# Optimization experiments

Hardware: AMD Instinct MI355X
Metric: run time of the kernel (lower is better)

Reference implementation:

```python
import jax, jax.numpy as jnp
import numpy as np

B, N, T, L = 4, 512, 288, 128
NEG_SLOPE = 0.2
TEMPERATURE = 0.2
CLAMP = 10.0
EPS = 1e-10


def setup_inputs() -> dict:
    key = jax.random.key(0)
    ks = jax.random.split(key, 6)
    s_in = 1.0 / np.sqrt(T)
    s_lat = 1.0 / np.sqrt(2 * L)
    s_b = 1.0 / np.sqrt(L)
    x = jax.random.normal(ks[0], (B, N, T), dtype=jnp.float32)
    W1 = jax.random.normal(ks[1], (L, T), dtype=jnp.float32) * s_in
    W2 = jax.random.normal(ks[2], (L, T), dtype=jnp.float32) * s_in
    Wp = jax.random.normal(ks[3], (L, 2 * L), dtype=jnp.float32) * s_lat
    Wb = jax.random.normal(ks[4], (L,), dtype=jnp.float32) * s_b
    noise = jnp.clip(jax.random.uniform(ks[5], (N, N), dtype=jnp.float32), 1e-6, 1.0 - 1e-6)
    return {
        "x": x,
        "W1": W1, "b1": jnp.zeros((L,), jnp.float32),
        "W2": W2, "b2": jnp.zeros((L,), jnp.float32),
        "Wp": Wp, "bp": jnp.zeros((L,), jnp.float32),
        "Wb": Wb, "bb": jnp.zeros((1,), jnp.float32),
        "noise": noise,
    }


def _leaky(v):
    return jnp.where(v >= 0, v, NEG_SLOPE * v)


def reference(x, W1, b1, W2, b2, Wp, bp, Wb, bb, noise):
    # per-node projections (B, N, L)
    x1 = _leaky(jnp.einsum('bnt,lt->bnl', x, W1) + b1)
    x2 = _leaky(jnp.einsum('bnt,lt->bnl', x, W2) + b2)
    # linear_para_latent(cat(x1_i, x2_j)) == x1_i @ Wp_a^T + x2_j @ Wp_b^T + bp
    Wp_a, Wp_b = Wp[:, :L], Wp[:, L:]
    s1 = jnp.einsum('bnl,ml->bnm', x1, Wp_a)  # (B, N, L_out)
    s2 = jnp.einsum('bnl,ml->bnm', x2, Wp_b)
    pair = s1[:, :, None, :] + s2[:, None, :, :] + bp  # (B, N, N, L)
    h = _leaky(pair)
    logits = jnp.einsum('bijl,l->bij', h, Wb) + bb[0]  # (B, N, N)
    p = jax.nn.sigmoid(logits).mean(axis=0)            # (N, N)
    p = p * (1.0 - jnp.eye(N, dtype=p.dtype))          # fill_diagonal_(0)
    # relaxed Bernoulli sample (binary concrete) with logit clamping
    logit_p = jnp.clip(jnp.log(p + EPS) - jnp.log1p(-p + EPS), -CLAMP, CLAMP)
    logistic = jnp.log(noise) - jnp.log1p(-noise)
    adj = jax.nn.sigmoid((logit_p + logistic) / TEMPERATURE)
    return adj
```

## Files before the change

### kernel.cpp

```cpp
#include <hip/hip_runtime.h>
#include <hip/hip_bf16.h>
#include <math.h>

#define NN 512
#define NT 288

__global__ __launch_bounds__(512) void kP(
    const float* __restrict__ x,
    const float* __restrict__ W1,
    const float* __restrict__ b1,
    const float* __restrict__ W2,
    const float* __restrict__ b2,
    const float* __restrict__ Wp,
    const float* __restrict__ bp,
    const float* __restrict__ Wb,
    const float* __restrict__ bb,
    float* __restrict__ S12,
    float* __restrict__ Aarr,
    float* __restrict__ Carr)
{
    __shared__ __align__(16) float xs[8 * NT];
    __shared__ __align__(16) float x12s[8 * 256];
    __shared__ __align__(16) float ph[8 * 256];

    const int t   = threadIdx.x;
    const int bn0 = blockIdx.x * 8;
    const int col = t & 255;
    const int kh  = t >> 8;

    for (int q = 0; q < 2; ++q) {
        int idx = q * 512 + t;
        if (idx < 576) {
            int row = idx / 72, c4 = idx % 72;
            *(float4*)&xs[row * NT + c4 * 4] =
                *(const float4*)&x[(size_t)(bn0 + row) * NT + c4 * 4];
        }
    }
    __syncthreads();

    const float* wrow = ((col < 128) ? (W1 + col * NT) : (W2 + (col - 128) * NT))
                        + kh * 144;
    const float bias1 = (col < 128) ? b1[col] : b2[col - 128];
    const int kb1 = kh * 144;

    float acc[8];
#pragma unroll
    for (int n = 0; n < 8; ++n) acc[n] = 0.0f;

    for (int k = 0; k < 144; k += 4) {
        float4 w = *(const float4*)(wrow + k);
#pragma unroll
        for (int n = 0; n < 8; ++n) {
            float4 xv = *(const float4*)&xs[n * NT + kb1 + k];
            acc[n] = fmaf(w.x, xv.x, acc[n]);
            acc[n] = fmaf(w.y, xv.y, acc[n]);
            acc[n] = fmaf(w.z, xv.z, acc[n]);
            acc[n] = fmaf(w.w, xv.w, acc[n]);
        }
    }
    if (kh) {
#pragma unroll
        for (int n = 0; n < 8; ++n) ph[n * 256 + col] = acc[n];
    }
    __syncthreads();
    if (!kh) {
#pragma unroll
        for (int n = 0; n < 8; ++n) {
            float v = acc[n] + ph[n * 256 + col] + bias1;
            x12s[n * 256 + col] = fmaxf(v, 0.2f * v);
        }
    }
    __syncthreads();

    const int koff = (col < 128) ? 0 : 128;
    const float* wprow = ((col < 128) ? (Wp + col * 256) : (Wp + (col - 128) * 256 + 128))
                         + kh * 64;
    const float bias2 = (col < 128) ? bp[col] : 0.0f;
    const int kb2 = koff + kh * 64;

    float acc2[8];
#pragma unroll
    for (int n = 0; n < 8; ++n) acc2[n] = 0.0f;

    for (int k = 0; k < 64; k += 4) {
        float4 w = *(const float4*)(wprow + k);
#pragma unroll
        for (int n = 0; n < 8; ++n) {
            float4 xv = *(const float4*)&x12s[n * 256 + kb2 + k];
            acc2[n] = fmaf(w.x, xv.x, acc2[n]);
            acc2[n] = fmaf(w.y, xv.y, acc2[n]);
            acc2[n] = fmaf(w.z, xv.z, acc2[n]);
            acc2[n] = fmaf(w.w, xv.w, acc2[n]);
        }
    }
    if (kh) {
#pragma unroll
        for (int n = 0; n < 8; ++n) ph[n * 256 + col] = acc2[n];
    }
    __syncthreads();

    float* s12s = xs;
    if (!kh) {
#pragma unroll
        for (int n = 0; n < 8; ++n) {
            float sv = acc2[n] + ph[n * 256 + col] + bias2;
            S12[(size_t)(bn0 + n) * 256 + col] = sv;
            s12s[n * 257 + col] = sv;
        }
    }
    __syncthreads();

    {
        int lane32 = t & 31;
        int n = (t >> 5) & 7;
        int isC = t >> 8;
        int base = isC ? 128 : 0;
        float sum = 0.0f;
#pragma unroll
        for (int s = 0; s < 4; ++s) {
            int j = lane32 + s * 32;
            sum = fmaf(s12s[n * 257 + base + j], Wb[j], sum);
        }
#pragma unroll
        for (int m = 16; m >= 1; m >>= 1)
            sum += __shfl_xor(sum, m, 32);
        if (lane32 == 0) {
            if (isC) Carr[bn0 + n] = 0.6f * sum;
            else     Aarr[bn0 + n] = 0.6f * sum + bb[0];
        }
    }
}

__global__ __launch_bounds__(512) void kQ(
    const float* __restrict__ S12,
    const float* __restrict__ Aarr,
    const float* __restrict__ Carr,
    const float* __restrict__ Wb,
    const float* __restrict__ noise,
    float* __restrict__ out)
{
    __shared__ __align__(16) float smem[32768];
    float* S1t = smem;
    float* S2t = smem + 16384;

    const int t = threadIdx.x;
    const int bx = blockIdx.x, by = blockIdx.y;

#pragma unroll
    for (int q = 0; q < 16; ++q) {
        int task = q * 512 + t;
        int isS2 = task >> 12;
        int r    = task & 4095;
        int bz   = r >> 10;
        int row  = (r >> 5) & 31;
        int c4   = r & 31;
        size_t src = (size_t)(bz * NN + (isS2 ? by : bx) * 32 + row) * 256
                     + (isS2 ? 128 : 0) + c4 * 4;
        float4 v = *(const float4*)&S12[src];
        float* dst = (isS2 ? S2t : S1t) + bz * 4096;
        int rw = row ^ ((c4 & 7) << 2);
        dst[(c4 * 4 + 0) * 32 + rw] = v.x;
        dst[(c4 * 4 + 1) * 32 + rw] = v.y;
        dst[(c4 * 4 + 2) * 32 + rw] = v.z;
        dst[(c4 * 4 + 3) * 32 + rw] = v.w;
    }
    __syncthreads();

    const int lh = t >> 8;
    const int bz = (t >> 6) & 3;
    const int s  = t & 63;
    const int i0 = (s >> 3) << 2, j0 = (s & 7) << 2;

    const float* S1b = S1t + bz * 4096 + lh * 64 * 32;
    const float* S2b = S2t + bz * 4096 + lh * 64 * 32;
    const float* wbp = Wb + lh * 64;

    float accv[16];
#pragma unroll
    for (int k = 0; k < 16; ++k) accv[k] = 0.0f;

    for (int l4 = 0; l4 < 16; ++l4) {
        const int sw = (l4 & 7) << 2;
        const int lrow = l4 * 4 * 32;
        float4 wv = *(const float4*)&wbp[l4 * 4];
        const float wl[4] = {wv.x, wv.y, wv.z, wv.w};
#pragma unroll
        for (int d = 0; d < 4; ++d) {
            float4 a = *(const float4*)&S1b[lrow + d * 32 + (i0 ^ sw)];
            float4 b = *(const float4*)&S2b[lrow + d * 32 + (j0 ^ sw)];
            float w = wl[d];
            float ai[4] = {a.x, a.y, a.z, a.w};
            float bj[4] = {b.x, b.y, b.z, b.w};
#pragma unroll
            for (int ii = 0; ii < 4; ++ii)
#pragma unroll
                for (int jj = 0; jj < 4; ++jj) {
                    float tv = ai[ii] + bj[jj];
                    accv[ii * 4 + jj] = fmaf(fabsf(tv), w, accv[ii * 4 + jj]);
                }
        }
    }

    float* red = smem;
    const int tid2 = t & 255;
    __syncthreads();
    if (lh) {
#pragma unroll
        for (int q = 0; q < 4; ++q) {
            float4 v = {accv[4 * q], accv[4 * q + 1], accv[4 * q + 2], accv[4 * q + 3]};
            *(float4*)&red[q * 1024 + tid2 * 4] = v;
        }
    }
    __syncthreads();

    float sig[16];
    if (!lh) {
#pragma unroll
        for (int q = 0; q < 4; ++q) {
            float4 v = *(const float4*)&red[q * 1024 + tid2 * 4];
            accv[4 * q]     += v.x;
            accv[4 * q + 1] += v.y;
            accv[4 * q + 2] += v.z;
            accv[4 * q + 3] += v.w;
        }
        float Av[4], Cv[4];
#pragma unroll
        for (int ii = 0; ii < 4; ++ii) Av[ii] = Aarr[bz * NN + bx * 32 + i0 + ii];
#pragma unroll
        for (int jj = 0; jj < 4; ++jj) Cv[jj] = Carr[bz * NN + by * 32 + j0 + jj];
#pragma unroll
        for (int ii = 0; ii < 4; ++ii)
#pragma unroll
            for (int jj = 0; jj < 4; ++jj) {
                float lg = Av[ii] + Cv[jj] + 0.4f * accv[ii * 4 + jj];
                sig[ii * 4 + jj] = 1.0f / (1.0f + expf(-lg));
            }
        float* redB = smem + 4096;
        if (bz) {
#pragma unroll
            for (int q = 0; q < 4; ++q) {
                float4 v = {sig[4 * q], sig[4 * q + 1], sig[4 * q + 2], sig[4 * q + 3]};
                *(float4*)&redB[(bz - 1) * 1024 + q * 256 + s * 4] = v;
            }
        }
    }
    __syncthreads();

    float* redB = smem + 4096;
    float* redP = smem + 7168;
    if (t < 64) {
#pragma unroll
        for (int bzz = 0; bzz < 3; ++bzz)
#pragma unroll
            for (int q = 0; q < 4; ++q) {
                float4 v = *(const float4*)&redB[bzz * 1024 + q * 256 + t * 4];
                sig[4 * q]     += v.x;
                sig[4 * q + 1] += v.y;
                sig[4 * q + 2] += v.z;
                sig[4 * q + 3] += v.w;
            }
#pragma unroll
        for (int q = 0; q < 4; ++q) {
            float4 v = {sig[4 * q], sig[4 * q + 1], sig[4 * q + 2], sig[4 * q + 3]};
            *(float4*)&redP[t * 16 + q * 4] = v;
        }
    }
    __syncthreads();

    if (t < 256) {
        int i   = t >> 3;
        int j0f = (t & 7) * 4;
        int sP  = (t >> 5) * 8 + (t & 7);
        int k0  = ((t >> 3) & 3) * 4;
        float4 pv4 = *(const float4*)&redP[sP * 16 + k0];
        float pv[4] = {pv4.x, pv4.y, pv4.z, pv4.w};

        int gi = bx * 32 + i;
        size_t base = (size_t)gi * NN + by * 32 + j0f;
        float4 nz = *(const float4*)&noise[base];
        float nv[4] = {nz.x, nz.y, nz.z, nz.w};

        float4 o;
        float* op = (float*)&o;
#pragma unroll
        for (int c = 0; c < 4; ++c) {
            float p = 0.25f * pv[c];
            int gj = by * 32 + j0f + c;
            if (gj == gi) p = 0.0f;
            float lp = logf(p + 1e-10f) - log1pf(-p + 1e-10f);
            lp = fminf(fmaxf(lp, -10.0f), 10.0f);
            float lgs = logf(nv[c]) - log1pf(-nv[c]);
            op[c] = 1.0f / (1.0f + expf(-(lp + lgs) * 5.0f));
        }
        *(float4*)&out[base] = o;
    }
}

extern "C" void kernel_launch(void* const* d_in, const int* in_sizes, int n_in,
                              void* d_out, int out_size, void* d_ws, size_t ws_size,
                              hipStream_t stream) {
    const float* x     = (const float*)d_in[0];
    const float* W1    = (const float*)d_in[1];
    const float* b1    = (const float*)d_in[2];
    const float* W2    = (const float*)d_in[3];
    const float* b2    = (const float*)d_in[4];
    const float* Wp    = (const float*)d_in[5];
    const float* bp    = (const float*)d_in[6];
    const float* Wb    = (const float*)d_in[7];
    const float* bb    = (const float*)d_in[8];
    const float* noise = (const float*)d_in[9];

    float* ws   = (float*)d_ws;
    float* S12  = ws;
    float* Aarr = ws + 524288;
    float* Carr = Aarr + 2048;

    kP<<<256, 512, 0, stream>>>(x, W1, b1, W2, b2, Wp, bp, Wb, bb,
                                S12, Aarr, Carr);
    kQ<<<dim3(16, 16), 512, 0, stream>>>(S12, Aarr, Carr, Wb, noise,
                                         (float*)d_out);
}
```

Measured before the change: 43.62 us.

## Pre-transpose projection weights for coalesced loads and read x directly from global

Adds a small kernel that transposes W1/W2 and the two halves of Wp into k-major layouts in workspace. The projection loops in kP can then load weights coalesced across threads instead of as per-thread strided float4 rows. The shared-memory staging of x is removed, and x is read as wavefront-uniform float4 loads straight from global memory. The cost is an extra kernel launch and a transpose pass on every call, plus x reads that now go through cache rather than LDS.

```diff
diff --git a/kernel.cpp b/kernel.cpp
--- a/kernel.cpp
+++ b/kernel.cpp
@@ -5,13 +5,29 @@
 #define NN 512
 #define NT 288
 
+__global__ __launch_bounds__(256) void kT(
+    const float* __restrict__ W1, const float* __restrict__ W2,
+    const float* __restrict__ Wp,
+    float* __restrict__ Wt, float* __restrict__ Wpt)
+{
+    int g = blockIdx.x * 256 + threadIdx.x;
+    if (g < 288 * 256) {
+        int k = g >> 8, col = g & 255;
+        Wt[g] = (col < 128) ? W1[col * 288 + k] : W2[(col - 128) * 288 + k];
+    } else {
+        int h = g - 288 * 256;
+        int k = h >> 8, col = h & 255;
+        Wpt[h] = (col < 128) ? Wp[col * 256 + k]
+                             : Wp[(col - 128) * 256 + 128 + k];
+    }
+}
+
 __global__ __launch_bounds__(512) void kP(
     const float* __restrict__ x,
-    const float* __restrict__ W1,
+    const float* __restrict__ Wt,
     const float* __restrict__ b1,
-    const float* __restrict__ W2,
     const float* __restrict__ b2,
-    const float* __restrict__ Wp,
+    const float* __restrict__ Wpt,
     const float* __restrict__ bp,
     const float* __restrict__ Wb,
     const float* __restrict__ bb,
@@ -19,45 +35,38 @@
     float* __restrict__ Aarr,
     float* __restrict__ Carr)
 {
-    __shared__ __align__(16) float xs[8 * NT];
     __shared__ __align__(16) float x12s[8 * 256];
     __shared__ __align__(16) float ph[8 * 256];
+    __shared__ __align__(16) float s12s[8 * 257];
 
     const int t   = threadIdx.x;
     const int bn0 = blockIdx.x * 8;
     const int col = t & 255;
     const int kh  = t >> 8;
 
-    for (int q = 0; q < 2; ++q) {
-        int idx = q * 512 + t;
-        if (idx < 576) {
-            int row = idx / 72, c4 = idx % 72;
-            *(float4*)&xs[row * NT + c4 * 4] =
-                *(const float4*)&x[(size_t)(bn0 + row) * NT + c4 * 4];
-        }
-    }
-    __syncthreads();
-
-    const float* wrow = ((col < 128) ? (W1 + col * NT) : (W2 + (col - 128) * NT))
-                        + kh * 144;
+    const float* xb  = x + (size_t)bn0 * NT + kh * 144;
+    const float* wtb = Wt + kh * 144 * 256 + col;
+
+    float acc[8];
+#pragma unroll
+    for (int n = 0; n < 8; ++n) acc[n] = 0.0f;
+
+    for (int k4 = 0; k4 < 36; ++k4) {
+        float w0 = wtb[(k4 * 4 + 0) * 256];
+        float w1 = wtb[(k4 * 4 + 1) * 256];
+        float w2 = wtb[(k4 * 4 + 2) * 256];
+        float w3 = wtb[(k4 * 4 + 3) * 256];
+#pragma unroll
+        for (int n = 0; n < 8; ++n) {
+            float4 xv = *(const float4*)&xb[n * NT + k4 * 4];
+            acc[n] = fmaf(w0, xv.x, acc[n]);
+            acc[n] = fmaf(w1, xv.y, acc[n]);
+            acc[n] = fmaf(w2, xv.z, acc[n]);
+            acc[n] = fmaf(w3, xv.w, acc[n]);
+        }
+    }
+
     const float bias1 = (col < 128) ? b1[col] : b2[col - 128];
-    const int kb1 = kh * 144;
-
-    float acc[8];
-#pragma unroll
-    for (int n = 0; n < 8; ++n) acc[n] = 0.0f;
-
-    for (int k = 0; k < 144; k += 4) {
-        float4 w = *(const float4*)(wrow + k);
-#pragma unroll
-        for (int n = 0; n < 8; ++n) {
-            float4 xv = *(const float4*)&xs[n * NT + kb1 + k];
-            acc[n] = fmaf(w.x, xv.x, acc[n]);
-            acc[n] = fmaf(w.y, xv.y, acc[n]);
-            acc[n] = fmaf(w.z, xv.z, acc[n]);
-            acc[n] = fmaf(w.w, xv.w, acc[n]);
-        }
-    }
     if (kh) {
 #pragma unroll
         for (int n = 0; n < 8; ++n) ph[n * 256 + col] = acc[n];
@@ -73,33 +82,34 @@
     __syncthreads();
 
     const int koff = (col < 128) ? 0 : 128;
-    const float* wprow = ((col < 128) ? (Wp + col * 256) : (Wp + (col - 128) * 256 + 128))
-                         + kh * 64;
+    const float* wptb = Wpt + kh * 64 * 256 + col;
+    const int kb2 = koff + kh * 64;
+
+    float acc2[8];
+#pragma unroll
+    for (int n = 0; n < 8; ++n) acc2[n] = 0.0f;
+
+    for (int k4 = 0; k4 < 16; ++k4) {
+        float w0 = wptb[(k4 * 4 + 0) * 256];
+        float w1 = wptb[(k4 * 4 + 1) * 256];
+        float w2 = wptb[(k4 * 4 + 2) * 256];
+        float w3 = wptb[(k4 * 4 + 3) * 256];
+#pragma unroll
+        for (int n = 0; n < 8; ++n) {
+            float4 xv = *(const float4*)&x12s[n * 256 + kb2 + k4 * 4];
+            acc2[n] = fmaf(w0, xv.x, acc2[n]);
+            acc2[n] = fmaf(w1, xv.y, acc2[n]);
+            acc2[n] = fmaf(w2, xv.z, acc2[n]);
+            acc2[n] = fmaf(w3, xv.w, acc2[n]);
+        }
+    }
+
     const float bias2 = (col < 128) ? bp[col] : 0.0f;
-    const int kb2 = koff + kh * 64;
-
-    float acc2[8];
-#pragma unroll
-    for (int n = 0; n < 8; ++n) acc2[n] = 0.0f;
-
-    for (int k = 0; k < 64; k += 4) {
-        float4 w = *(const float4*)(wprow + k);
-#pragma unroll
-        for (int n = 0; n < 8; ++n) {
-            float4 xv = *(const float4*)&x12s[n * 256 + kb2 + k];
-            acc2[n] = fmaf(w.x, xv.x, acc2[n]);
-            acc2[n] = fmaf(w.y, xv.y, acc2[n]);
-            acc2[n] = fmaf(w.z, xv.z, acc2[n]);
-            acc2[n] = fmaf(w.w, xv.w, acc2[n]);
-        }
-    }
     if (kh) {
 #pragma unroll
         for (int n = 0; n < 8; ++n) ph[n * 256 + col] = acc2[n];
     }
     __syncthreads();
-
-    float* s12s = xs;
     if (!kh) {
 #pragma unroll
         for (int n = 0; n < 8; ++n) {
@@ -314,8 +324,11 @@
     float* S12  = ws;
     float* Aarr = ws + 524288;
     float* Carr = Aarr + 2048;
-
-    kP<<<256, 512, 0, stream>>>(x, W1, b1, W2, b2, Wp, bp, Wb, bb,
+    float* Wt   = Carr + 2048;
+    float* Wpt  = Wt + 73728;
+
+    kT<<<416, 256, 0, stream>>>(W1, W2, Wp, Wt, Wpt);
+    kP<<<256, 512, 0, stream>>>(x, Wt, b1, b2, Wpt, bp, Wb, bb,
                                 S12, Aarr, Carr);
     kQ<<<dim3(16, 16), 512, 0, stream>>>(S12, Aarr, Carr, Wb, noise,
                                          (float*)d_out);
```

Measured after the change: 105.1 us. 141% more time.

## Pre-transpose weights for coalesced loads and split pair kernel across 1024 threads

Applied to the files above, without the earlier changes.

Adds a kernel that rearranges W1/W2 and Wp into a k4-major interleaved layout, so each thread's float4 weight load in kP is coalesced across columns. kP now reads x and the intermediate x12 straight from global memory (x12 goes through a global scratch buffer) instead of staging them in shared memory. kQ moves to 1024 threads, splitting the latent reduction four ways instead of two, with a wider shared-memory reduction. This costs an extra launch and transposes the weights on every call, and adds global round trips for x12.

```diff
diff --git a/kernel.cpp b/kernel.cpp
--- a/kernel.cpp
+++ b/kernel.cpp
@@ -5,59 +5,69 @@
 #define NN 512
 #define NT 288
 
+__global__ __launch_bounds__(256) void kT(
+    const float* __restrict__ W1, const float* __restrict__ W2,
+    const float* __restrict__ Wp,
+    float* __restrict__ Wt2, float* __restrict__ Wpt2)
+{
+    int g = blockIdx.x * 256 + threadIdx.x;
+    if (g < 73728) {
+        int k4 = g >> 10, col = (g >> 2) & 255, d = g & 3;
+        int k = k4 * 4 + d;
+        Wt2[g] = (col < 128) ? W1[col * 288 + k] : W2[(col - 128) * 288 + k];
+    } else {
+        int h = g - 73728;
+        int k4 = h >> 10, col = (h >> 2) & 255, d = h & 3;
+        int k = k4 * 4 + d;
+        Wpt2[h] = (col < 128) ? Wp[col * 256 + k]
+                              : Wp[(col - 128) * 256 + 128 + k];
+    }
+}
+
 __global__ __launch_bounds__(512) void kP(
     const float* __restrict__ x,
-    const float* __restrict__ W1,
+    const float* __restrict__ Wt2,
     const float* __restrict__ b1,
-    const float* __restrict__ W2,
     const float* __restrict__ b2,
-    const float* __restrict__ Wp,
+    const float* __restrict__ Wpt2,
     const float* __restrict__ bp,
     const float* __restrict__ Wb,
     const float* __restrict__ bb,
     float* __restrict__ S12,
     float* __restrict__ Aarr,
-    float* __restrict__ Carr)
+    float* __restrict__ Carr,
+    float* __restrict__ x12g)
 {
-    __shared__ __align__(16) float xs[8 * NT];
-    __shared__ __align__(16) float x12s[8 * 256];
     __shared__ __align__(16) float ph[8 * 256];
+    __shared__ __align__(16) float s12s[8 * 257];
 
     const int t   = threadIdx.x;
     const int bn0 = blockIdx.x * 8;
     const int col = t & 255;
     const int kh  = t >> 8;
 
-    for (int q = 0; q < 2; ++q) {
-        int idx = q * 512 + t;
-        if (idx < 576) {
-            int row = idx / 72, c4 = idx % 72;
-            *(float4*)&xs[row * NT + c4 * 4] =
-                *(const float4*)&x[(size_t)(bn0 + row) * NT + c4 * 4];
-        }
-    }
-    __syncthreads();
-
-    const float* wrow = ((col < 128) ? (W1 + col * NT) : (W2 + (col - 128) * NT))
-                        + kh * 144;
-    const float bias1 = (col < 128) ? b1[col] : b2[col - 128];
-    const int kb1 = kh * 144;
+    const int kb1 = __builtin_amdgcn_readfirstlane(kh * 144);
+    const float* xu  = x + (size_t)bn0 * NT;
+    const float* wtb = Wt2 + (size_t)(kh * 36) * 1024 + col * 4;
 
     float acc[8];
 #pragma unroll
     for (int n = 0; n < 8; ++n) acc[n] = 0.0f;
 
-    for (int k = 0; k < 144; k += 4) {
-        float4 w = *(const float4*)(wrow + k);
+#pragma unroll 2
+    for (int k4 = 0; k4 < 36; ++k4) {
+        float4 w = *(const float4*)&wtb[k4 * 1024];
 #pragma unroll
         for (int n = 0; n < 8; ++n) {
-            float4 xv = *(const float4*)&xs[n * NT + kb1 + k];
+            float4 xv = *(const float4*)&xu[n * NT + kb1 + k4 * 4];
             acc[n] = fmaf(w.x, xv.x, acc[n]);
             acc[n] = fmaf(w.y, xv.y, acc[n]);
             acc[n] = fmaf(w.z, xv.z, acc[n]);
             acc[n] = fmaf(w.w, xv.w, acc[n]);
         }
     }
+
+    const float bias1 = (col < 128) ? b1[col] : b2[col - 128];
     if (kh) {
 #pragma unroll
         for (int n = 0; n < 8; ++n) ph[n * 256 + col] = acc[n];
@@ -67,26 +77,26 @@
 #pragma unroll
         for (int n = 0; n < 8; ++n) {
             float v = acc[n] + ph[n * 256 + col] + bias1;
-            x12s[n * 256 + col] = fmaxf(v, 0.2f * v);
-        }
-    }
-    __syncthreads();
-
-    const int koff = (col < 128) ? 0 : 128;
-    const float* wprow = ((col < 128) ? (Wp + col * 256) : (Wp + (col - 128) * 256 + 128))
-                         + kh * 64;
+            x12g[(size_t)(bn0 + n) * 256 + col] = fmaxf(v, 0.2f * v);
+        }
+    }
+    __syncthreads();
+
+    const int kb2 = __builtin_amdgcn_readfirstlane(((col < 128) ? 0 : 128) + kh * 64);
+    const float* x2u = x12g + (size_t)bn0 * 256;
+    const float* wpb = Wpt2 + (size_t)(kh * 16) * 1024 + col * 4;
     const float bias2 = (col < 128) ? bp[col] : 0.0f;
-    const int kb2 = koff + kh * 64;
 
     float acc2[8];
 #pragma unroll
     for (int n = 0; n < 8; ++n) acc2[n] = 0.0f;
 
-    for (int k = 0; k < 64; k += 4) {
-        float4 w = *(const float4*)(wprow + k);
+#pragma unroll 2
+    for (int k4 = 0; k4 < 16; ++k4) {
+        float4 w = *(const float4*)&wpb[k4 * 1024];
 #pragma unroll
         for (int n = 0; n < 8; ++n) {
-            float4 xv = *(const float4*)&x12s[n * 256 + kb2 + k];
+            float4 xv = *(const float4*)&x2u[n * 256 + kb2 + k4 * 4];
             acc2[n] = fmaf(w.x, xv.x, acc2[n]);
             acc2[n] = fmaf(w.y, xv.y, acc2[n]);
             acc2[n] = fmaf(w.z, xv.z, acc2[n]);
@@ -99,7 +109,6 @@
     }
     __syncthreads();
 
-    float* s12s = xs;
     if (!kh) {
 #pragma unroll
         for (int n = 0; n < 8; ++n) {
@@ -131,7 +140,7 @@
     }
 }
 
-__global__ __launch_bounds__(512) void kQ(
+__global__ __launch_bounds__(1024) void kQ(
     const float* __restrict__ S12,
     const float* __restrict__ Aarr,
     const float* __restrict__ Carr,
@@ -147,8 +156,8 @@
     const int bx = blockIdx.x, by = blockIdx.y;
 
 #pragma unroll
-    for (int q = 0; q < 16; ++q) {
-        int task = q * 512 + t;
+    for (int q = 0; q < 8; ++q) {
+        int task = q * 1024 + t;
         int isS2 = task >> 12;
         int r    = task & 4095;
         int bz   = r >> 10;
@@ -166,20 +175,20 @@
     }
     __syncthreads();
 
-    const int lh = t >> 8;
+    const int lq = t >> 8;
     const int bz = (t >> 6) & 3;
     const int s  = t & 63;
     const int i0 = (s >> 3) << 2, j0 = (s & 7) << 2;
 
-    const float* S1b = S1t + bz * 4096 + lh * 64 * 32;
-    const float* S2b = S2t + bz * 4096 + lh * 64 * 32;
-    const float* wbp = Wb + lh * 64;
+    const float* S1b = S1t + bz * 4096 + lq * 32 * 32;
+    const float* S2b = S2t + bz * 4096 + lq * 32 * 32;
+    const float* wbp = Wb + lq * 32;
 
     float accv[16];
 #pragma unroll
     for (int k = 0; k < 16; ++k) accv[k] = 0.0f;
 
-    for (int l4 = 0; l4 < 16; ++l4) {
+    for (int l4 = 0; l4 < 8; ++l4) {
         const int sw = (l4 & 7) << 2;
         const int lrow = l4 * 4 * 32;
         float4 wv = *(const float4*)&wbp[l4 * 4];
@@ -204,25 +213,28 @@
     float* red = smem;
     const int tid2 = t & 255;
     __syncthreads();
-    if (lh) {
+    if (lq) {
 #pragma unroll
         for (int q = 0; q < 4; ++q) {
             float4 v = {accv[4 * q], accv[4 * q + 1], accv[4 * q + 2], accv[4 * q + 3]};
-            *(float4*)&red[q * 1024 + tid2 * 4] = v;
+            *(float4*)&red[(lq - 1) * 4096 + q * 1024 + tid2 * 4] = v;
         }
     }
     __syncthreads();
 
     float sig[16];
-    if (!lh) {
-#pragma unroll
-        for (int q = 0; q < 4; ++q) {
-            float4 v = *(const float4*)&red[q * 1024 + tid2 * 4];
-            accv[4 * q]     += v.x;
-            accv[4 * q + 1] += v.y;
-            accv[4 * q + 2] += v.z;
-            accv[4 * q + 3] += v.w;
-        }
+    float* redB = smem + 12288;
+    if (!lq) {
+#pragma unroll
+        for (int p = 0; p < 3; ++p)
+#pragma unroll
+            for (int q = 0; q < 4; ++q) {
+                float4 v = *(const float4*)&red[p * 4096 + q * 1024 + tid2 * 4];
+                accv[4 * q]     += v.x;
+                accv[4 * q + 1] += v.y;
+                accv[4 * q + 2] += v.z;
+                accv[4 * q + 3] += v.w;
+            }
         float Av[4], Cv[4];
 #pragma unroll
         for (int ii = 0; ii < 4; ++ii) Av[ii] = Aarr[bz * NN + bx * 32 + i0 + ii];
@@ -235,7 +247,6 @@
                 float lg = Av[ii] + Cv[jj] + 0.4f * accv[ii * 4 + jj];
                 sig[ii * 4 + jj] = 1.0f / (1.0f + expf(-lg));
             }
-        float* redB = smem + 4096;
         if (bz) {
 #pragma unroll
             for (int q = 0; q < 4; ++q) {
@@ -246,8 +257,7 @@
     }
     __syncthreads();
 
-    float* redB = smem + 4096;
-    float* redP = smem + 7168;
+    float* redP = smem + 15360;
     if (t < 64) {
 #pragma unroll
         for (int bzz = 0; bzz < 3; ++bzz)
@@ -314,9 +324,13 @@
     float* S12  = ws;
     float* Aarr = ws + 524288;
     float* Carr = Aarr + 2048;
-
-    kP<<<256, 512, 0, stream>>>(x, W1, b1, W2, b2, Wp, bp, Wb, bb,
-                                S12, Aarr, Carr);
-    kQ<<<dim3(16, 16), 512, 0, stream>>>(S12, Aarr, Carr, Wb, noise,
-                                         (float*)d_out);
+    float* Wt2  = Carr + 2048;
+    float* Wpt2 = Wt2 + 73728;
+    float* x12g = Wpt2 + 32768;
+
+    kT<<<416, 256, 0, stream>>>(W1, W2, Wp, Wt2, Wpt2);
+    kP<<<256, 512, 0, stream>>>(x, Wt2, b1, b2, Wpt2, bp, Wb, bb,
+                                S12, Aarr, Carr, x12g);
+    kQ<<<dim3(16, 16), 1024, 0, stream>>>(S12, Aarr, Carr, Wb, noise,
+                                          (float*)d_out);
 }
```

New measurement: 45.31 us. +3.9%, slower.
